# Performance work log

Hardware: AMD Instinct MI355X
Metric: run time of the kernel (lower is better)

## Reference

```python
import jax, jax.numpy as jnp
import numpy as np

EPS = 1e-5
KF = 3  # kernel_field

def _layernorm(x, g, b):
    m = jnp.mean(x, axis=-1, keepdims=True)
    v = jnp.var(x, axis=-1, keepdims=True)
    return (x - m) * jax.lax.rsqrt(v + EPS) * g + b

def _sai2token(buf, W_mlp):
    # buf: [b, c, a, h, w] -> tokens [h*w, b*a, spa_dim]
    b, c, a, h, w = buf.shape
    x = buf.transpose(0, 2, 1, 3, 4).reshape(b * a, c, h, w)
    xp = jnp.pad(x, ((0, 0), (0, 0), (1, 1), (1, 1)))
    # torch F.unfold ordering: channel slowest, then kernel (i, j)
    patches = jnp.stack([xp[:, :, i:i + h, j:j + w] for i in range(KF) for j in range(KF)], axis=2)
    tok = patches.reshape(b * a, c * KF * KF, h * w).transpose(2, 0, 1)  # [hw, ba, c*9]
    return tok @ W_mlp

def _attention(x, Wqkv, Wproj, bproj, Wl, bl, Ww, bw, lamb, num_heads):
    B, N, C = x.shape
    hd = C // num_heads
    scale = hd ** -0.5
    qkv = (x @ Wqkv).reshape(B, N, 3, num_heads, hd).transpose(2, 0, 3, 1, 4)
    q, k, v = qkv[0] * scale, qkv[1], qkv[2]  # each [B, H, N, hd]
    attn = jnp.einsum('bhnd,bhmd->bhnm', q, k)
    # talking-heads mix before softmax (proj_l)
    attn = jnp.einsum('bhnm,gh->bgnm', attn, Wl) + bl[None, :, None, None]
    attn = jax.nn.softmax(attn, axis=-1)
    # talking-heads mix after softmax (proj_w)
    attn = jnp.einsum('bhnm,gh->bgnm', attn, Ww) + bw[None, :, None, None]
    # attnscale: attn_d + (attn - attn_d) * (1 + lamb_h)
    attn_d = 1.0 / N
    attn = attn_d + (attn - attn_d) * (1.0 + lamb[None, :, None, None])
    out = jnp.einsum('bhnm,bhmd->bhnd', attn, v).transpose(0, 2, 1, 3).reshape(B, N, C)
    return out @ Wproj + bproj


def setup_inputs() -> dict:
    key = jax.random.key(0)
    ks = jax.random.split(key, 20)
    b, c, a, h, w = 4, 128, 25, 32, 32
    D = 2 * c           # spa_dim = 256
    H = 8               # num_heads
    cin = c * KF * KF   # 1152
    f32 = jnp.float32
    def nrm(k, shp, s=0.02):
        return (jax.random.normal(k, shp, dtype=f32) * s)
    return {
        'buffer': jax.random.normal(ks[0], (b, c, a, h, w), dtype=f32),
        'spa_position': jax.random.normal(ks[1], (b, c, a, h, w), dtype=f32) * 0.02,
        'W_mlp': nrm(ks[2], (cin, D)),
        'g1': jnp.ones((D,), f32), 'b1': jnp.zeros((D,), f32),
        'Wqkv': nrm(ks[3], (D, 3 * D)),
        'Wproj': nrm(ks[4], (D, D)), 'bproj': jnp.zeros((D,), f32),
        'Wl': nrm(ks[5], (H, H), 0.3), 'bl': jnp.zeros((H,), f32),
        'Ww': nrm(ks[6], (H, H), 0.3), 'bw': jnp.zeros((H,), f32),
        'lamb': jnp.zeros((H,), f32),
        'g2': jnp.ones((D,), f32), 'b2': jnp.zeros((D,), f32),
        'W1': nrm(ks[7], (D, 2 * D)),
        'W2': nrm(ks[8], (2 * D, D)),
        'Wconv': nrm(ks[9], (c, D)),
    }


def reference(buffer, spa_position, W_mlp, g1, b1, Wqkv, Wproj, bproj,
              Wl, bl, Ww, bw, lamb, g2, b2, W1, W2, Wconv):
    b, c, a, h, w = buffer.shape
    num_heads = Wl.shape[0]
    # gen_mask is computed in the original forward but never used -> omitted.
    spa_token = _sai2token(buffer, W_mlp)          # [hw, ba, D]
    spa_PE = _sai2token(spa_position, W_mlp)       # [hw, ba, D]
    x = _layernorm(spa_token + spa_PE, g1, b1)
    spa_token = _attention(x, Wqkv, Wproj, bproj, Wl, bl, Ww, bw, lamb, num_heads) + spa_token
    # feed-forward: LN -> Linear(D,2D,no bias) -> ReLU -> Linear(2D,D,no bias)
    y = _layernorm(spa_token, g2, b2)
    y = jax.nn.relu(y @ W1) @ W2
    spa_token = y + spa_token
    # Token2SAI: '(h w) (b a) c -> b c a h w' then 1x1x1 Conv3d (D -> c, no bias)
    D = spa_token.shape[-1]
    buf = spa_token.reshape(h, w, b, a, D).transpose(2, 4, 3, 0, 1)  # [b, D, a, h, w]
    out = jnp.einsum('bdahw,od->boahw', buf, Wconv)
    return out
```

## Files before the change

### kernel.cpp

```cpp
#include <hip/hip_runtime.h>
#include <hip/hip_bf16.h>

typedef unsigned short u16;
typedef unsigned int u32;
typedef short bf16x8 __attribute__((ext_vector_type(8)));
typedef float f32x4 __attribute__((ext_vector_type(4)));

#define MFMA(a,b,c) __builtin_amdgcn_mfma_f32_16x16x32_bf16((a),(b),(c),0,0,0)

__device__ __forceinline__ float bf2f(u16 v) { u32 t = ((u32)v) << 16; float f; __builtin_memcpy(&f, &t, 4); return f; }
__device__ __forceinline__ u16 f2bf(float f) { u32 x; __builtin_memcpy(&x, &f, 4); u32 r = (x + 0x7FFFu + ((x >> 16) & 1u)) >> 16; return (u16)r; }
__device__ __forceinline__ float san(float v) { return (fabsf(v) < 1e30f) ? v : 0.f; }
__device__ __forceinline__ float lde(const void* p, long i, int flag) {
    return flag ? bf2f(((const u16*)p)[i]) : ((const float*)p)[i];
}

__device__ __forceinline__ bf16x8 ldfrag8(const u16* p) {
    union { bf16x8 v; uint2 q[2]; } u;
    u.q[0] = *(const uint2*)p;
    u.q[1] = *(const uint2*)(p + 4);
    return u.v;
}
__device__ __forceinline__ bf16x8 ldfrag16(const u16* p) {
    union { bf16x8 v; uint4 q; } u;
    u.q = *(const uint4*)p;
    return u.v;
}
__device__ __forceinline__ bf16x8 ldtail(const u16* p) {
    union { bf16x8 v; uint2 q[2]; } u;
    u.q[0] = *(const uint2*)p;
    u.q[1].x = 0; u.q[1].y = 0;
    return u.v;
}

__device__ __forceinline__ void gload16(const u16* g, u16* l) {
    __builtin_amdgcn_global_load_lds(
        (const __attribute__((address_space(1))) u16*)g,
        (__attribute__((address_space(3))) u16*)l, 16, 0, 0);
}

__global__ void detect_dtype(const u32* __restrict__ g1w, int* __restrict__ flag) {
    if (threadIdx.x == 0 && blockIdx.x == 0)
        *flag = (g1w[0] == 0x3F800000u) ? 0 : 1;
}

__global__ __launch_bounds__(256) void fill_sentinel(float* __restrict__ out, int n) {
    int i = blockIdx.x * 256 + threadIdx.x;
    if (i < n) out[i] = 2.0f;
}

__global__ __launch_bounds__(256) void prep_weights(
    const void* __restrict__ Wmlp, const void* __restrict__ Wqkv,
    const void* __restrict__ Wproj, const void* __restrict__ W1,
    const void* __restrict__ W2, const void* __restrict__ Wconv,
    const void* __restrict__ g1, const void* __restrict__ b1,
    const void* __restrict__ g2, const void* __restrict__ b2,
    const void* __restrict__ bproj, const void* __restrict__ Wl,
    const void* __restrict__ Ww, const void* __restrict__ bl,
    const void* __restrict__ bw, const void* __restrict__ lamb,
    u16* __restrict__ Wt1, u16* __restrict__ WqkvT, u16* __restrict__ WprojT,
    u16* __restrict__ W1T, u16* __restrict__ W2T, u16* __restrict__ WconvF,
    float* __restrict__ PRM, u16* __restrict__ ZEROB, const int* __restrict__ flagp)
{
    int i = blockIdx.x * 256 + threadIdx.x;
    int flag = *flagp;
    if (i < 294912) {
        int d = i / 1152, kp = i % 1152;
        int pos9 = kp >> 7, ch = kp & 127;
        Wt1[i] = f2bf(lde(Wmlp, (ch * 9 + pos9) * 256 + d, flag));
    } else if (i < 491520) {
        int j = i - 294912; int jj = j / 256, kk = j % 256;
        WqkvT[j] = f2bf(lde(Wqkv, kk * 768 + jj, flag));
    } else if (i < 557056) {
        int j = i - 491520; int jj = j / 256, kk = j % 256;
        WprojT[j] = f2bf(lde(Wproj, kk * 256 + jj, flag));
    } else if (i < 688128) {
        int j = i - 557056; int jj = j / 256, kk = j % 256;
        W1T[j] = f2bf(lde(W1, kk * 512 + jj, flag));
    } else if (i < 819200) {
        int j = i - 688128; int jj = j / 512, kk = j % 512;
        W2T[j] = f2bf(lde(W2, kk * 256 + jj, flag));
    } else if (i < 851968) {
        int j = i - 819200;
        WconvF[j] = f2bf(lde(Wconv, j, flag));
    } else if (i < 853400) {
        int idx = i - 851968;
        float v;
        if      (idx < 256)  v = lde(g1,    idx,        flag);
        else if (idx < 512)  v = lde(b1,    idx - 256,  flag);
        else if (idx < 768)  v = lde(g2,    idx - 512,  flag);
        else if (idx < 1024) v = lde(b2,    idx - 768,  flag);
        else if (idx < 1280) v = lde(bproj, idx - 1024, flag);
        else if (idx < 1344) v = lde(Wl,    idx - 1280, flag);
        else if (idx < 1408) v = lde(Ww,    idx - 1344, flag);
        else if (idx < 1416) v = lde(bl,    idx - 1408, flag);
        else if (idx < 1424) v = lde(bw,    idx - 1416, flag);
        else                 v = lde(lamb,  idx - 1424, flag);
        PRM[idx] = v;
    } else if (i < 853464) {
        ZEROB[i - 853400] = 0;
    }
}

__global__ __launch_bounds__(256) void make_tokens(
    const void* __restrict__ buf, const void* __restrict__ pos,
    u16* __restrict__ tb, u16* __restrict__ ts, const int* __restrict__ flagp)
{
    __shared__ u16 t0[64 * 66];
    __shared__ u16 t1[64 * 66];
    int flag = *flagp;
    int nba = blockIdx.z; int bb = nba / 25, aa = nba % 25;
    int ch0 = blockIdx.y * 64, p0 = blockIdx.x * 64;
    int lane = threadIdx.x & 63, grp = threadIdx.x >> 6;
    for (int cc = grp; cc < 64; cc += 4) {
        long gi = ((long)(bb * 128 + ch0 + cc) * 25 + aa) * 1024 + p0 + lane;
        float v0 = lde(buf, gi, flag);
        float v1 = lde(pos, gi, flag);
        t0[cc * 66 + lane] = f2bf(v0);
        t1[cc * 66 + lane] = f2bf(v0 + v1);
    }
    __syncthreads();
    for (int pp = grp; pp < 64; pp += 4) {
        size_t go = (size_t)(p0 + pp) * 12800 + (size_t)nba * 128 + ch0 + lane;
        tb[go] = t0[lane * 66 + pp];
        ts[go] = t1[lane * 66 + pp];
    }
}

__global__ __launch_bounds__(256) void gemm_conv(
    const u16* __restrict__ Tin, const u16* __restrict__ Wt, u16* __restrict__ C,
    const u16* __restrict__ ZB)
{
    __shared__ u16 As[128 * 64];
    __shared__ u16 Bs[128 * 64];
    const int m0 = blockIdx.y * 128, n0 = blockIdx.x * 128;
    const int tid = threadIdx.x;
    const int lane = tid & 63, wave = tid >> 6;
    const int wr = wave >> 1, wc = wave & 1;
    const int l15 = lane & 15, l4 = lane >> 4;
    const int colk = (tid & 7) * 8;
    int ys[4], xs[4];
    const u16* Ab[4];
#pragma unroll
    for (int i = 0; i < 4; ++i) {
        int row = m0 + i * 32 + (tid >> 3);
        int pp = row / 100, snb = row - pp * 100;
        ys[i] = pp >> 5; xs[i] = pp & 31;
        Ab[i] = Tin + (size_t)snb * 128 + colk;
    }
    const u16* Bg = Wt + (size_t)(n0 + (tid >> 3)) * 1152 + colk;
    u16* Asw = &As[(wave * 8) * 64];
    u16* Bsw = &Bs[(wave * 8) * 64];
    f32x4 acc[4][4] = {};

    auto stage = [&](int k0) {
        int pos9 = k0 >> 7, ch0 = k0 & 127;
        int dy = pos9 / 3 - 1, dx = pos9 % 3 - 1;
#pragma unroll
        for (int i = 0; i < 4; ++i) {
            int yy = ys[i] + dy, xx = xs[i] + dx;
            bool ok = ((unsigned)yy < 32u) && ((unsigned)xx < 32u);
            const u16* src = ok ? (Ab[i] + (size_t)(yy * 32 + xx) * 12800 + ch0) : ZB;
            gload16(src, Asw + i * 32 * 64);
            gload16(Bg + (size_t)i * 32 * 1152 + k0, Bsw + i * 32 * 64);
        }
    };

    stage(0);
    int k0 = 0;
    while (true) {
        __syncthreads();
#pragma unroll
        for (int ks = 0; ks < 2; ++ks) {
            const int koff = ks * 32 + l4 * 8;
            bf16x8 af[4], bq[4];
#pragma unroll
            for (int q = 0; q < 4; ++q) {
                af[q] = ldfrag16(&As[(wr * 64 + q * 16 + l15) * 64 + koff]);
                bq[q] = ldfrag16(&Bs[(wc * 64 + q * 16 + l15) * 64 + koff]);
            }
#pragma unroll
            for (int mi = 0; mi < 4; ++mi)
#pragma unroll
                for (int ni = 0; ni < 4; ++ni)
                    acc[mi][ni] = MFMA(af[mi], bq[ni], acc[mi][ni]);
        }
        k0 += 64;
        if (k0 >= 1152) break;
        __syncthreads();
        stage(k0);
    }
#pragma unroll
    for (int mi = 0; mi < 4; ++mi)
#pragma unroll
        for (int ni = 0; ni < 4; ++ni) {
            int col = n0 + wc * 64 + ni * 16 + l15;
#pragma unroll
            for (int r = 0; r < 4; ++r) {
                int row = m0 + wr * 64 + mi * 16 + l4 * 4 + r;
                C[(size_t)row * 256 + col] = f2bf(san(acc[mi][ni][r]));
            }
        }
}

template<int MODE>
__global__ __launch_bounds__(256) void gemm_bt(
    const u16* __restrict__ A, const u16* __restrict__ Bt, u16* __restrict__ C,
    int M, int N, int K,
    const float* __restrict__ bias, const u16* __restrict__ res,
    float* __restrict__ Cf)
{
    __shared__ u16 As[128 * 64];
    __shared__ u16 Bs[128 * 64];
    const int m0 = blockIdx.y * 128, n0 = blockIdx.x * 128;
    const int tid = threadIdx.x;
    const int lane = tid & 63, wave = tid >> 6;
    const int wr = wave >> 1, wc = wave & 1;
    const int l15 = lane & 15, l4 = lane >> 4;
    const u16* Ag = A + (size_t)(m0 + (tid >> 3)) * K + (tid & 7) * 8;
    const u16* Bg = Bt + (size_t)(n0 + (tid >> 3)) * K + (tid & 7) * 8;
    u16* Asw = &As[(wave * 8) * 64];
    u16* Bsw = &Bs[(wave * 8) * 64];
    const size_t rstep = (size_t)32 * K;
    f32x4 acc[4][4] = {};

#pragma unroll
    for (int i = 0; i < 4; ++i) {
        gload16(Ag + (size_t)i * rstep, Asw + i * 32 * 64);
        gload16(Bg + (size_t)i * rstep, Bsw + i * 32 * 64);
    }
    int k0 = 0;
    while (true) {
        __syncthreads();
#pragma unroll
        for (int ks = 0; ks < 2; ++ks) {
            const int koff = ks * 32 + l4 * 8;
            bf16x8 af[4], bq[4];
#pragma unroll
            for (int q = 0; q < 4; ++q) {
                af[q] = ldfrag16(&As[(wr * 64 + q * 16 + l15) * 64 + koff]);
                bq[q] = ldfrag16(&Bs[(wc * 64 + q * 16 + l15) * 64 + koff]);
            }
#pragma unroll
            for (int mi = 0; mi < 4; ++mi)
#pragma unroll
                for (int ni = 0; ni < 4; ++ni)
                    acc[mi][ni] = MFMA(af[mi], bq[ni], acc[mi][ni]);
        }
        k0 += 64;
        if (k0 >= K) break;
        __syncthreads();
#pragma unroll
        for (int i = 0; i < 4; ++i) {
            gload16(Ag + k0 + (size_t)i * rstep, Asw + i * 32 * 64);
            gload16(Bg + k0 + (size_t)i * rstep, Bsw + i * 32 * 64);
        }
    }
#pragma unroll
    for (int mi = 0; mi < 4; ++mi)
#pragma unroll
        for (int ni = 0; ni < 4; ++ni) {
            int col = n0 + wc * 64 + ni * 16 + l15;
#pragma unroll
            for (int r = 0; r < 4; ++r) {
                int row = m0 + wr * 64 + mi * 16 + l4 * 4 + r;
                float v = san(acc[mi][ni][r]);
                if (MODE == 0) {
                    C[(size_t)row * N + col] = f2bf(v);
                } else if (MODE == 1) {
                    v += bias[col] + bf2f(res[(size_t)row * N + col]);
                    C[(size_t)row * N + col] = f2bf(san(v));
                } else if (MODE == 2) {
                    C[(size_t)row * N + col] = f2bf(fmaxf(v, 0.f));
                } else if (MODE == 3) {
                    v += bf2f(res[(size_t)row * N + col]);
                    int pp = row / 100, nb = row % 100;
                    C[((size_t)nb * 1024 + pp) * 256 + col] = f2bf(san(v));
                } else {
                    int nb = col >> 10, pp = col & 1023;
                    int bb = nb / 25, aa = nb % 25;
                    Cf[(((size_t)bb * 128 + row) * 25 + aa) * 1024 + pp] = v;
                }
            }
        }
}

__global__ __launch_bounds__(256) void ln_kernel(
    const u16* __restrict__ in, const float* __restrict__ g,
    const float* __restrict__ b, u16* __restrict__ out)
{
    int wave = threadIdx.x >> 6, lane = threadIdx.x & 63;
    size_t row = (size_t)blockIdx.x * 4 + wave;
    const u16* rp = in + row * 256 + lane * 4;
    uint2 rv = *(const uint2*)rp;
    float x0 = bf2f(rv.x & 0xffff), x1 = bf2f(rv.x >> 16);
    float x2 = bf2f(rv.y & 0xffff), x3 = bf2f(rv.y >> 16);
    float s = x0 + x1 + x2 + x3;
    float ss = x0 * x0 + x1 * x1 + x2 * x2 + x3 * x3;
    for (int off = 32; off > 0; off >>= 1) { s += __shfl_xor(s, off); ss += __shfl_xor(ss, off); }
    float mean = s * (1.f / 256.f);
    float var = ss * (1.f / 256.f) - mean * mean;
    float inv = rsqrtf(fmaxf(var, 0.f) + 1e-5f);
    float4 gv = *(const float4*)(g + lane * 4);
    float4 bv = *(const float4*)(b + lane * 4);
    u16 o0 = f2bf(san((x0 - mean) * inv * gv.x + bv.x));
    u16 o1 = f2bf(san((x1 - mean) * inv * gv.y + bv.y));
    u16 o2 = f2bf(san((x2 - mean) * inv * gv.z + bv.z));
    u16 o3 = f2bf(san((x3 - mean) * inv * gv.w + bv.w));
    uint2 ov; ov.x = (u32)o0 | ((u32)o1 << 16); ov.y = (u32)o2 | ((u32)o3 << 16);
    *(uint2*)(out + row * 256 + lane * 4) = ov;
}

__global__ __launch_bounds__(512) void attn_fused(
    const u16* __restrict__ qkv, const float* __restrict__ prm,
    u16* __restrict__ AO)
{
    const int MSS = 104;
    const int MSV = 100;
    __shared__ u16 S4s[128 * 104];
    __shared__ u16 vT[256 * 100];
    __shared__ float cl_s[64], ww_s[64];
    __shared__ float bl_s[8], bw_s[8], lam_s[8];
    int p = blockIdx.x;
    int tid = threadIdx.x;
    int lane = tid & 63, wave = tid >> 6;
    int l15 = lane & 15, l4 = lane >> 4;
    if (tid < 64) { cl_s[tid] = prm[1280 + tid] * 0.17677669529663687f; ww_s[tid] = prm[1344 + tid]; }
    else if (tid < 72) { int j = tid - 64; bl_s[j] = prm[1408 + j]; bw_s[j] = prm[1416 + j]; lam_s[j] = prm[1424 + j]; }
    const u16* base = qkv + (size_t)p * 76800;

    {
        int mg = tid >> 5;
        int dv0 = (tid & 31) * 8;
        int rot = tid & 7;
        for (int mb = 0; mb < 100; mb += 16) {
            int m = mb + mg;
            if (m < 100) {
                union { uint4 q; u16 e[8]; } u;
                u.q = *(const uint4*)(base + 512 + (size_t)m * 768 + dv0);
#pragma unroll
                for (int j = 0; j < 8; ++j) {
                    int jj = (j + rot) & 7;
                    vT[(dv0 + jj) * MSV + m] = u.e[jj];
                }
            }
        }
    }
    __syncthreads();

    for (int t = 0; t < 7; ++t) {
        int n0 = t * 16;

        if (wave < 7) {
            int nq = n0 + l15; if (nq > 99) nq = 99;
            bf16x8 qf[8];
#pragma unroll
            for (int h = 0; h < 8; ++h)
                qf[h] = ldfrag16(base + nq * 768 + h * 32 + l4 * 8);
            int m0 = wave * 16;
            int mk = m0 + l15; if (mk > 99) mk = 99;
            f32x4 S[8];
#pragma unroll
            for (int h = 0; h < 8; ++h) {
                bf16x8 kf = ldfrag16(base + mk * 768 + 256 + h * 32 + l4 * 8);
                f32x4 z = {};
                S[h] = MFMA(qf[h], kf, z);
            }
            int mm = m0 + l15;
            if (mm < 100) {
#pragma unroll
                for (int g = 0; g < 8; ++g) {
                    float bgl = bl_s[g];
#pragma unroll
                    for (int r = 0; r < 4; ++r) {
                        float s2 = bgl;
#pragma unroll
                        for (int h = 0; h < 8; ++h) s2 += cl_s[g * 8 + h] * S[h][r];
                        s2 = fminf(fmaxf(s2, -80.f), 80.f);
                        S4s[(g * 16 + l4 * 4 + r) * MSS + mm] = f2bf(s2);
                    }
                }
            }
        }
        __syncthreads();

        {
            int row = tid >> 2, sub = tid & 3;
            u32* rp32 = (u32*)(S4s + row * MSS);
            float v[26];
#pragma unroll
            for (int i = 0; i < 13; ++i) {
                u32 d = rp32[sub + i * 4];
                v[2 * i]     = bf2f((u16)(d & 0xffff));
                v[2 * i + 1] = bf2f((u16)(d >> 16));
            }
            if (sub >= 2) { v[24] = -1e30f; v[25] = -1e30f; }
            float m0 = v[0], m1 = v[1];
#pragma unroll
            for (int j = 2; j < 26; j += 2) {
                m0 = fmaxf(m0, v[j]); m1 = fmaxf(m1, v[j + 1]);
            }
            float mx = fmaxf(m0, m1);
            mx = fmaxf(mx, __shfl_xor(mx, 1));
            mx = fmaxf(mx, __shfl_xor(mx, 2));
            float s0 = 0.f, s1 = 0.f;
#pragma unroll
            for (int j = 0; j < 26; j += 2) {
                v[j]     = __expf(v[j]     - mx); s0 += v[j];
                v[j + 1] = __expf(v[j + 1] - mx); s1 += v[j + 1];
            }
            float sum = s0 + s1;
            sum += __shfl_xor(sum, 1);
            sum += __shfl_xor(sum, 2);
            float inv = 1.f / sum;
#pragma unroll
            for (int i = 0; i < 13; ++i) {
                u32 d = (u32)f2bf(v[2 * i] * inv) | ((u32)f2bf(v[2 * i + 1] * inv) << 16);
                rp32[sub + i * 4] = d;
            }
        }
        __syncthreads();

        for (int idx = tid; idx < 832; idx += 512) {
            int nl = idx / 52, mc = idx - (idx / 52) * 52;
            float P0[8], P1[8];
#pragma unroll
            for (int g = 0; g < 8; ++g) {
                u32 d = *(const u32*)&S4s[(g * 16 + nl) * MSS + mc * 2];
                P0[g] = bf2f((u16)(d & 0xffff));
                P1[g] = bf2f((u16)(d >> 16));
            }
#pragma unroll
            for (int gp = 0; gp < 8; ++gp) {
                float a = bw_s[gp], b = bw_s[gp];
#pragma unroll
                for (int g = 0; g < 8; ++g) {
                    float w = ww_s[gp * 8 + g];
                    a += w * P0[g]; b += w * P1[g];
                }
                float lg = 1.f + lam_s[gp];
                a = 0.01f + (a - 0.01f) * lg;
                b = 0.01f + (b - 0.01f) * lg;
                u32 d = (u32)f2bf(san(a)) | ((u32)f2bf(san(b)) << 16);
                *(u32*)&S4s[(gp * 16 + nl) * MSS + mc * 2] = d;
            }
        }
        __syncthreads();

        {
            bf16x8 zz = {};
            int g = wave;
            bf16x8 pa[4];
#pragma unroll
            for (int ks = 0; ks < 3; ++ks)
                pa[ks] = ldfrag8(&S4s[(g * 16 + l15) * MSS + ks * 32 + l4 * 8]);
            pa[3] = (l4 == 0) ? ldtail(&S4s[(g * 16 + l15) * MSS + 96]) : zz;
#pragma unroll
            for (int dh = 0; dh < 2; ++dh) {
                int vd = g * 32 + dh * 16 + l15;
                f32x4 acc = {};
#pragma unroll
                for (int ks = 0; ks < 3; ++ks) {
                    bf16x8 vb = ldfrag8(&vT[vd * MSV + ks * 32 + l4 * 8]);
                    acc = MFMA(pa[ks], vb, acc);
                }
                bf16x8 vb3 = (l4 == 0) ? ldtail(&vT[vd * MSV + 96]) : zz;
                acc = MFMA(pa[3], vb3, acc);
#pragma unroll
                for (int r = 0; r < 4; ++r) {
                    int n = n0 + l4 * 4 + r;
                    if (n < 100)
                        AO[((size_t)p * 100 + n) * 256 + g * 32 + dh * 16 + l15] = f2bf(san(acc[r]));
                }
            }
        }
        __syncthreads();
    }
}

extern "C" void kernel_launch(void* const* d_in, const int* in_sizes, int n_in,
                              void* d_out, int out_size, void* d_ws, size_t ws_size,
                              hipStream_t stream) {
    (void)in_sizes; (void)n_in;
    const void* buffer  = d_in[0];
    const void* spa_pos = d_in[1];
    const void* W_mlp   = d_in[2];
    const void* g1      = d_in[3];
    const void* b1      = d_in[4];
    const void* Wqkv    = d_in[5];
    const void* Wproj   = d_in[6];
    const void* bproj   = d_in[7];
    const void* Wl      = d_in[8];
    const void* bl      = d_in[9];
    const void* Ww      = d_in[10];
    const void* bw      = d_in[11];
    const void* lamb    = d_in[12];
    const void* g2      = d_in[13];
    const void* b2      = d_in[14];
    const void* W1      = d_in[15];
    const void* W2      = d_in[16];
    const void* Wconv   = d_in[17];

    if (ws_size < 263856320ULL) {
        fill_sentinel<<<(out_size + 255) / 256, 256, 0, stream>>>((float*)d_out, out_size);
        return;
    }

    char* ws = (char*)d_ws;
    u16* TINB  = (u16*)(ws + 0);
    u16* TINS  = (u16*)(ws + 26214400);
    u16* X     = (u16*)(ws + 0);
    u16* AO    = (u16*)(ws + 0);
    u16* Y0    = (u16*)(ws + 0);
    u16* T0    = (u16*)(ws + 52428800);
    u16* SPA3  = (u16*)(ws + 52428800);
    u16* T1    = (u16*)(ws + 104857600);
    u16* QKV   = (u16*)(ws + 104857600);
    u16* SPA2  = (u16*)(ws + 104857600);
    u16* H1    = (u16*)(ws + 157286400);
    u16* WT1   = (u16*)(ws + 262144000);
    u16* WQKVT = (u16*)(ws + 262733824);
    u16* WPROJT= (u16*)(ws + 263127040);
    u16* W1T   = (u16*)(ws + 263258112);
    u16* W2T   = (u16*)(ws + 263520256);
    u16* WCONVF= (u16*)(ws + 263782400);
    float* PRM = (float*)(ws + 263847936);
    int* FLAG  = (int*)(ws + 263856128);
    u16* ZB    = (u16*)(ws + 263856192);

    detect_dtype<<<1, 64, 0, stream>>>((const u32*)g1, FLAG);
    prep_weights<<<3334, 256, 0, stream>>>(W_mlp, Wqkv, Wproj, W1, W2, Wconv,
                                           g1, b1, g2, b2, bproj, Wl, Ww, bl, bw, lamb,
                                           WT1, WQKVT, WPROJT, W1T, W2T, WCONVF, PRM, ZB, FLAG);
    make_tokens<<<dim3(16, 2, 100), 256, 0, stream>>>(buffer, spa_pos, TINB, TINS, FLAG);
    gemm_conv<<<dim3(2, 800), 256, 0, stream>>>(TINB, WT1, T0, ZB);
    gemm_conv<<<dim3(2, 800), 256, 0, stream>>>(TINS, WT1, T1, ZB);
    ln_kernel<<<25600, 256, 0, stream>>>(T1, PRM + 0, PRM + 256, X);
    gemm_bt<0><<<dim3(6, 800), 256, 0, stream>>>(X, WQKVT, QKV, 102400, 768, 256, nullptr, nullptr, nullptr);
    attn_fused<<<1024, 512, 0, stream>>>(QKV, PRM, AO);
    gemm_bt<1><<<dim3(2, 800), 256, 0, stream>>>(AO, WPROJT, SPA2, 102400, 256, 256, PRM + 1024, T0, nullptr);
    ln_kernel<<<25600, 256, 0, stream>>>(SPA2, PRM + 512, PRM + 768, Y0);
    gemm_bt<2><<<dim3(4, 800), 256, 0, stream>>>(Y0, W1T, H1, 102400, 512, 256, nullptr, nullptr, nullptr);
    gemm_bt<3><<<dim3(2, 800), 256, 0, stream>>>(H1, W2T, SPA3, 102400, 256, 512, nullptr, SPA2, nullptr);
    gemm_bt<4><<<dim3(800, 1), 256, 0, stream>>>(WCONVF, SPA3, nullptr, 128, 102400, 256, nullptr, nullptr, (float*)d_out);
}
```

Measured before the change: 905.5 us.

## Process two query tiles per iteration in attention with 1024-thread blocks

```diff
diff --git a/kernel.cpp b/kernel.cpp
--- a/kernel.cpp
+++ b/kernel.cpp
@@ -311,13 +311,13 @@
     *(uint2*)(out + row * 256 + lane * 4) = ov;
 }
 
-__global__ __launch_bounds__(512) void attn_fused(
+__global__ __launch_bounds__(1024) void attn_fused(
     const u16* __restrict__ qkv, const float* __restrict__ prm,
     u16* __restrict__ AO)
 {
     const int MSS = 104;
     const int MSV = 100;
-    __shared__ u16 S4s[128 * 104];
+    __shared__ u16 S4s[2 * 128 * 104];
     __shared__ u16 vT[256 * 100];
     __shared__ float cl_s[64], ww_s[64];
     __shared__ float bl_s[8], bw_s[8], lam_s[8];
@@ -333,7 +333,7 @@
         int mg = tid >> 5;
         int dv0 = (tid & 31) * 8;
         int rot = tid & 7;
-        for (int mb = 0; mb < 100; mb += 16) {
+        for (int mb = 0; mb < 100; mb += 32) {
             int m = mb + mg;
             if (m < 100) {
                 union { uint4 q; u16 e[8]; } u;
@@ -348,16 +348,18 @@
     }
     __syncthreads();
 
-    for (int t = 0; t < 7; ++t) {
-        int n0 = t * 16;
-
-        if (wave < 7) {
-            int nq = n0 + l15; if (nq > 99) nq = 99;
+    for (int t0 = 0; t0 < 7; t0 += 2) {
+        const int ntile = (t0 == 6) ? 1 : 2;
+
+        if (wave < 7 * ntile) {
+            int ti = (wave >= 7) ? 1 : 0;
+            int u = wave - ti * 7;
+            int nq = (t0 + ti) * 16 + l15; if (nq > 99) nq = 99;
             bf16x8 qf[8];
 #pragma unroll
             for (int h = 0; h < 8; ++h)
                 qf[h] = ldfrag16(base + nq * 768 + h * 32 + l4 * 8);
-            int m0 = wave * 16;
+            int m0 = u * 16;
             int mk = m0 + l15; if (mk > 99) mk = 99;
             f32x4 S[8];
 #pragma unroll
@@ -377,7 +379,7 @@
 #pragma unroll
                         for (int h = 0; h < 8; ++h) s2 += cl_s[g * 8 + h] * S[h][r];
                         s2 = fminf(fmaxf(s2, -80.f), 80.f);
-                        S4s[(g * 16 + l4 * 4 + r) * MSS + mm] = f2bf(s2);
+                        S4s[(ti * 128 + g * 16 + l4 * 4 + r) * MSS + mm] = f2bf(s2);
                     }
                 }
             }
@@ -386,47 +388,52 @@
 
         {
             int row = tid >> 2, sub = tid & 3;
-            u32* rp32 = (u32*)(S4s + row * MSS);
-            float v[26];
-#pragma unroll
-            for (int i = 0; i < 13; ++i) {
-                u32 d = rp32[sub + i * 4];
-                v[2 * i]     = bf2f((u16)(d & 0xffff));
-                v[2 * i + 1] = bf2f((u16)(d >> 16));
-            }
-            if (sub >= 2) { v[24] = -1e30f; v[25] = -1e30f; }
-            float m0 = v[0], m1 = v[1];
-#pragma unroll
-            for (int j = 2; j < 26; j += 2) {
-                m0 = fmaxf(m0, v[j]); m1 = fmaxf(m1, v[j + 1]);
-            }
-            float mx = fmaxf(m0, m1);
-            mx = fmaxf(mx, __shfl_xor(mx, 1));
-            mx = fmaxf(mx, __shfl_xor(mx, 2));
-            float s0 = 0.f, s1 = 0.f;
-#pragma unroll
-            for (int j = 0; j < 26; j += 2) {
-                v[j]     = __expf(v[j]     - mx); s0 += v[j];
-                v[j + 1] = __expf(v[j + 1] - mx); s1 += v[j + 1];
-            }
-            float sum = s0 + s1;
-            sum += __shfl_xor(sum, 1);
-            sum += __shfl_xor(sum, 2);
-            float inv = 1.f / sum;
-#pragma unroll
-            for (int i = 0; i < 13; ++i) {
-                u32 d = (u32)f2bf(v[2 * i] * inv) | ((u32)f2bf(v[2 * i + 1] * inv) << 16);
-                rp32[sub + i * 4] = d;
-            }
-        }
-        __syncthreads();
-
-        for (int idx = tid; idx < 832; idx += 512) {
-            int nl = idx / 52, mc = idx - (idx / 52) * 52;
+            if (row < 128 * ntile) {
+                u32* rp32 = (u32*)(S4s + row * MSS);
+                float v[26];
+#pragma unroll
+                for (int i = 0; i < 13; ++i) {
+                    u32 d = rp32[sub + i * 4];
+                    v[2 * i]     = bf2f((u16)(d & 0xffff));
+                    v[2 * i + 1] = bf2f((u16)(d >> 16));
+                }
+                if (sub >= 2) { v[24] = -1e30f; v[25] = -1e30f; }
+                float m0 = v[0], m1 = v[1];
+#pragma unroll
+                for (int j = 2; j < 26; j += 2) {
+                    m0 = fmaxf(m0, v[j]); m1 = fmaxf(m1, v[j + 1]);
+                }
+                float mx = fmaxf(m0, m1);
+                mx = fmaxf(mx, __shfl_xor(mx, 1));
+                mx = fmaxf(mx, __shfl_xor(mx, 2));
+                float s0 = 0.f, s1 = 0.f;
+#pragma unroll
+                for (int j = 0; j < 26; j += 2) {
+                    v[j]     = __expf(v[j]     - mx); s0 += v[j];
+                    v[j + 1] = __expf(v[j + 1] - mx); s1 += v[j + 1];
+                }
+                float sum = s0 + s1;
+                sum += __shfl_xor(sum, 1);
+                sum += __shfl_xor(sum, 2);
+                float inv = 1.f / sum;
+#pragma unroll
+                for (int i = 0; i < 13; ++i) {
+                    u32 d = (u32)f2bf(v[2 * i] * inv) | ((u32)f2bf(v[2 * i + 1] * inv) << 16);
+                    rp32[sub + i * 4] = d;
+                }
+            }
+        }
+        __syncthreads();
+
+        for (int idx = tid; idx < 832 * ntile; idx += 1024) {
+            int ti = (idx >= 832) ? 1 : 0;
+            int rem = idx - ti * 832;
+            int nl = rem / 52, mc = rem - nl * 52;
+            u16* sb = S4s + (size_t)ti * 128 * MSS;
             float P0[8], P1[8];
 #pragma unroll
             for (int g = 0; g < 8; ++g) {
-                u32 d = *(const u32*)&S4s[(g * 16 + nl) * MSS + mc * 2];
+                u32 d = *(const u32*)&sb[(g * 16 + nl) * MSS + mc * 2];
                 P0[g] = bf2f((u16)(d & 0xffff));
                 P1[g] = bf2f((u16)(d >> 16));
             }
@@ -442,19 +449,21 @@
                 a = 0.01f + (a - 0.01f) * lg;
                 b = 0.01f + (b - 0.01f) * lg;
                 u32 d = (u32)f2bf(san(a)) | ((u32)f2bf(san(b)) << 16);
-                *(u32*)&S4s[(gp * 16 + nl) * MSS + mc * 2] = d;
-            }
-        }
-        __syncthreads();
-
-        {
+                *(u32*)&sb[(gp * 16 + nl) * MSS + mc * 2] = d;
+            }
+        }
+        __syncthreads();
+
+        if (wave < 8 * ntile) {
             bf16x8 zz = {};
-            int g = wave;
+            int ti = wave >> 3, g = wave & 7;
+            int n0 = (t0 + ti) * 16;
+            const u16* srow = S4s + ((size_t)ti * 128 + g * 16 + l15) * MSS;
             bf16x8 pa[4];
 #pragma unroll
             for (int ks = 0; ks < 3; ++ks)
-                pa[ks] = ldfrag8(&S4s[(g * 16 + l15) * MSS + ks * 32 + l4 * 8]);
-            pa[3] = (l4 == 0) ? ldtail(&S4s[(g * 16 + l15) * MSS + 96]) : zz;
+                pa[ks] = ldfrag8(srow + ks * 32 + l4 * 8);
+            pa[3] = (l4 == 0) ? ldtail(srow + 96) : zz;
 #pragma unroll
             for (int dh = 0; dh < 2; ++dh) {
                 int vd = g * 32 + dh * 16 + l15;
@@ -537,7 +546,7 @@
     gemm_conv<<<dim3(2, 800), 256, 0, stream>>>(TINS, WT1, T1, ZB);
     ln_kernel<<<25600, 256, 0, stream>>>(T1, PRM + 0, PRM + 256, X);
     gemm_bt<0><<<dim3(6, 800), 256, 0, stream>>>(X, WQKVT, QKV, 102400, 768, 256, nullptr, nullptr, nullptr);
-    attn_fused<<<1024, 512, 0, stream>>>(QKV, PRM, AO);
+    attn_fused<<<1024, 1024, 0, stream>>>(QKV, PRM, AO);
     gemm_bt<1><<<dim3(2, 800), 256, 0, stream>>>(AO, WPROJT, SPA2, 102400, 256, 256, PRM + 1024, T0, nullptr);
     ln_kernel<<<25600, 256, 0, stream>>>(SPA2, PRM + 512, PRM + 768, Y0);
     gemm_bt<2><<<dim3(4, 800), 256, 0, stream>>>(Y0, W1T, H1, 102400, 512, 256, nullptr, nullptr, nullptr);
```

New measurement: 1.697 ms. 87.4% more time.
